# Kernel optimization log

Measured on AMD Instinct MI355X. Metric: run time of the kernel, lower is better.

## Reference

```python
import jax, jax.numpy as jnp
import numpy as np

B, N, IN, E, OUT = 4, 128, 256, 128, 128
EPS = 1e-5
NEG = -1.0e9


def _ln(x, s, o):
    m = x.mean(-1, keepdims=True)
    v = ((x - m) ** 2).mean(-1, keepdims=True)
    return s * jax.lax.rsqrt(v + EPS) * (x - m) + o


def setup_inputs() -> dict:
    key = jax.random.key(0)
    ks = jax.random.split(key, 30)

    def w(k, i, o):
        return (jax.random.normal(k, (i, o), jnp.float32) / np.sqrt(i)).astype(jnp.float32)

    z_dense = jax.random.normal(ks[0], (B, N, IN), jnp.float32)
    e_dense = jax.random.normal(ks[1], (B, N, N, E), jnp.float32)
    graph_fts = jax.random.normal(ks[2], (B, IN // 2), jnp.float32)
    lengths = jax.random.randint(ks[3], (B,), N // 2, N + 1)
    mask = jnp.arange(N)[None, :] < lengths[:, None]  # (B,N) bool
    adj = jax.random.uniform(ks[4], (B, N, N)) < 0.3
    adj = (adj | jnp.eye(N, dtype=bool)[None]) & mask[:, :, None] & mask[:, None, :]
    return dict(
        z_dense=z_dense, e_dense=e_dense, graph_fts=graph_fts, mask=mask, adj_mat=adj,
        Wt1=w(ks[5], IN, 8), Wt2=w(ks[6], IN, 8), Wt3=w(ks[7], IN, 8),
        We1=w(ks[8], E, 8), We2=w(ks[9], E, 8), We3=w(ks[10], E, 8),
        Wg=w(ks[11], IN // 2, 8),
        Wm1=w(ks[12], IN, OUT), Wm2=w(ks[13], IN, OUT), Wme=w(ks[14], E, OUT), Wmg=w(ks[15], E, OUT),
        ln1_s=jnp.ones((OUT,), jnp.float32), ln1_o=jnp.zeros((OUT,), jnp.float32),
        Wmlp1=w(ks[16], OUT, OUT),
        ln2_s=jnp.ones((OUT,), jnp.float32), ln2_o=jnp.zeros((OUT,), jnp.float32),
        Wmlp2=w(ks[17], OUT, OUT),
        WU1=w(ks[18], IN, OUT), WU2=w(ks[19], OUT, OUT), WU3=w(ks[20], 8, OUT),
        lnf_s=jnp.ones((OUT,), jnp.float32), lnf_o=jnp.zeros((OUT,), jnp.float32),
    )


def reference(z_dense, e_dense, graph_fts, mask, adj_mat,
              Wt1, Wt2, Wt3, We1, We2, We3, Wg,
              Wm1, Wm2, Wme, Wmg,
              ln1_s, ln1_o, Wmlp1, ln2_s, ln2_o, Wmlp2,
              WU1, WU2, WU3, lnf_s, lnf_o):
    mN = mask[..., None]  # (B,N,1)
    # --- triplet messages ---
    tri_1 = jnp.where(mN, z_dense @ Wt1, 0.0)  # (B,N,8)
    tri_2 = jnp.where(mN, z_dense @ Wt2, 0.0)
    tri_3 = jnp.where(mN, z_dense @ Wt3, 0.0)
    tri_e1 = e_dense @ We1  # (B,N,N,8)
    tri_e2 = e_dense @ We2
    tri_e3 = e_dense @ We3
    tri_g = graph_fts @ Wg  # (B,8)
    # (B,N,N,N,8) 7-way broadcast sum (axes: b, i, j, k)
    tri = (tri_1[:, :, None, None, :] + tri_2[:, None, :, None, :] + tri_3[:, None, None, :, :]
           + tri_e1[:, :, :, None, :] + tri_e2[:, :, None, :, :] + tri_e3[:, None, :, :, :]
           + tri_g[:, None, None, None, :])
    msk_tri = mask[:, None, None, :] | mask[:, None, :, None] | mask[:, :, None, None]
    tri = jnp.where(msk_tri[..., None], tri, NEG)
    tri_pooled = tri.max(axis=1)  # (B,N,N,8) -- max over first node axis
    tri_msgs = jax.nn.relu(tri_pooled @ WU3)  # (B,N,N,OUT)

    # --- pairwise messages ---
    msg_1 = jnp.where(mN, z_dense @ Wm1, 0.0)  # (B,N,OUT)
    msg_2 = jnp.where(mN, z_dense @ Wm2, 0.0)
    msg_e = jnp.where(adj_mat[..., None], e_dense @ Wme, 0.0)  # (B,N,N,OUT)
    msg_g = graph_fts @ Wmg  # (B,OUT)
    msgs = msg_1[:, None, :, :] + msg_2[:, :, None, :] + msg_e + msg_g[:, None, None, :]
    # M[-1]: [LN, ReLU, Linear] x2
    x = jax.nn.relu(_ln(msgs, ln1_s, ln1_o)) @ Wmlp1
    x = jax.nn.relu(_ln(x, ln2_s, ln2_o)) @ Wmlp2
    msgs = jnp.where(adj_mat[..., None], x, NEG).max(axis=1)  # (B,N,OUT)

    ret = _ln(z_dense @ WU1 + msgs @ WU2, lnf_s, lnf_o)  # (B,N,OUT)
    return ret, msgs, tri_msgs
```

## Files before the change

### kernel.cpp

```cpp
#include <hip/hip_runtime.h>

#define BN   4
#define NN   128
#define INF  256
#define EF   128
#define OUTF 128
#define EPSF 1e-5f
#define NEGF -998244352.0f

typedef __attribute__((ext_vector_type(8))) short short8;
typedef __attribute__((ext_vector_type(4))) float f32x4;

#define MFMA16(a, b, c) __builtin_amdgcn_mfma_f32_16x16x32_bf16(a, b, c, 0, 0, 0)

__device__ __forceinline__ unsigned short f2bf(float f) {
    unsigned u = __float_as_uint(f);
    u += 0x7fffu + ((u >> 16) & 1u);
    return (unsigned short)(u >> 16);
}
__device__ __forceinline__ unsigned pack2(float a, float b) {
    return (unsigned)f2bf(a) | ((unsigned)f2bf(b) << 16);
}

constexpr size_t TRI1 = 0;
constexpr size_t TRI2 = 4096;
constexpr size_t TRI3 = 8192;
constexpr size_t MSG1 = 12288;
constexpr size_t MSG2 = 77824;
constexpr size_t ZWU1 = 143360;
constexpr size_t TRIG = 208896;
constexpr size_t MSGG = 209920;
constexpr size_t E1T  = 210944;
constexpr size_t E2T  = 735232;
constexpr size_t E3N  = 1259520;
constexpr size_t PREPF = 1914880;

constexpr int W1T_OFF  = 0;
constexpr int W2T_OFF  = 16384;
constexpr int WMET_OFF = 32768;

constexpr size_t O_RET = 0;
constexpr size_t O_MSG = 65536;
constexpr size_t O_TRI = 131072;

__device__ __forceinline__ int detect_int(const void* mask) {
    const unsigned char* m = (const unsigned char*)mask;
    return (m[1] | m[2] | m[3]) == 0 ? 1 : 0;
}
__device__ __forceinline__ bool rdbool(const void* p, size_t idx, int isInt) {
    if (isInt) return ((const int*)p)[idx] != 0;
    return ((const unsigned char*)p)[idx] != 0;
}

__global__ __launch_bounds__(256, 4) void k_pre(
    const float* __restrict__ z, const float* __restrict__ e, const void* __restrict__ mask,
    const float* __restrict__ Wt1, const float* __restrict__ Wt2, const float* __restrict__ Wt3,
    const float* __restrict__ Wm1, const float* __restrict__ Wm2, const float* __restrict__ WU1,
    const float* __restrict__ g, const float* __restrict__ Wg, const float* __restrict__ Wmg,
    const float* __restrict__ W1, const float* __restrict__ W2, const float* __restrict__ Wme,
    const float* __restrict__ We1, const float* __restrict__ We2, const float* __restrict__ We3,
    float* __restrict__ ws, unsigned short* __restrict__ prep)
{
    int bx = blockIdx.x, tid = threadIdx.x;
    __shared__ __align__(16) unsigned char smem[128 * 136 * 2];

    if (bx < 512) {
        unsigned short* Ab = (unsigned short*)smem;
        int bi = bx;
        int b = bi >> 7, i = bi & 127;
        int lane = tid & 63, w = tid >> 6, q = lane >> 4, n = lane & 15;
        {
            int half = lane >> 5, c4 = (lane & 31) * 4;
            #pragma unroll
            for (int it = 0; it < 16; it++) {
                int row = 32 * w + 2 * it + half;
                float4 v = *(const float4*)(e + (size_t)bi * 16384 + (size_t)row * 128 + c4);
                unsigned* dst = (unsigned*)&Ab[row * 136 + c4];
                dst[0] = pack2(v.x, v.y);
                dst[1] = pack2(v.z, v.w);
            }
        }
        float t1v;
        {
            int c = lane & 7, kk = lane >> 3;
            const float* zr = z + (size_t)bi * INF;
            float s = 0.f;
            #pragma unroll
            for (int m = 0; m < 32; m++) s = fmaf(zr[kk * 32 + m], Wt1[(kk * 32 + m) * 8 + c], s);
            s += __shfl_xor(s, 8, 64);
            s += __shfl_xor(s, 16, 64);
            s += __shfl_xor(s, 32, 64);
            int isInt = detect_int(mask);
            t1v = rdbool(mask, bi, isInt) ? s : 0.f;
        }
        short8 bfrag[4][2];
        {
            #pragma unroll
            for (int t = 0; t < 2; t++) {
                int col = 16 * t + n;
                const float* Wsel = (col < 8) ? We1 : (col < 16 ? We2 : We3);
                int csel = col & 7;
                float mval = (col < 24) ? 1.f : 0.f;
                #pragma unroll
                for (int ks = 0; ks < 4; ks++) {
                    union { short8 s; unsigned short u[8]; } tmp;
                    #pragma unroll
                    for (int jj = 0; jj < 8; jj++) {
                        int k = ks * 32 + q * 8 + jj;
                        tmp.u[jj] = f2bf(Wsel[k * 8 + csel] * mval);
                    }
                    bfrag[ks][t] = tmp.s;
                }
            }
        }
        __builtin_amdgcn_wave_barrier();

        f32x4 ac2[2][2];
        #pragma unroll
        for (int rt = 0; rt < 2; rt++)
            #pragma unroll
            for (int t = 0; t < 2; t++) ac2[rt][t] = 0.f;
        #pragma unroll
        for (int ks = 0; ks < 4; ks++) {
            int k0 = ks * 32 + q * 8;
            short8 a0 = *(const short8*)&Ab[(32 * w + n) * 136 + k0];
            short8 a1 = *(const short8*)&Ab[(32 * w + 16 + n) * 136 + k0];
            #pragma unroll
            for (int t = 0; t < 2; t++) {
                ac2[0][t] = MFMA16(a0, bfrag[ks][t], ac2[0][t]);
                ac2[1][t] = MFMA16(a1, bfrag[ks][t], ac2[1][t]);
            }
        }
        #pragma unroll
        for (int rt = 0; rt < 2; rt++)
            #pragma unroll
            for (int reg = 0; reg < 4; reg++) {
                int row = 32 * w + 16 * rt + 4 * q + reg;
                float v0 = ac2[rt][0][reg];
                if (n < 8) ws[E1T + ((size_t)(b * 128 + row) * 128 + i) * 8 + n] = v0 + t1v;
                else       ws[E2T + ((size_t)(b * 128 + row) * 128 + i) * 8 + (n - 8)] = v0;
                if (n < 8) ws[E3N + ((size_t)bi * 128 + row) * 8 + n] = ac2[rt][1][reg];
            }
        return;
    }
    if (bx < 1024) {
        int bn = bx - 512;
        int isInt = detect_int(mask);
        float* zr = (float*)smem;
        zr[tid] = z[(size_t)bn * INF + tid];
        __syncthreads();
        float mk = rdbool(mask, bn, isInt) ? 1.f : 0.f;
        for (int idx = tid; idx < 408; idx += 256) {
            const float* W; int c; size_t dst; int width; bool msk;
            if (idx < 8)        { W = Wt1; c = idx;       dst = TRI1 + (size_t)bn * 8;   width = 8;   msk = true;  }
            else if (idx < 16)  { W = Wt2; c = idx - 8;   dst = TRI2 + (size_t)bn * 8;   width = 8;   msk = true;  }
            else if (idx < 24)  { W = Wt3; c = idx - 16;  dst = TRI3 + (size_t)bn * 8;   width = 8;   msk = true;  }
            else if (idx < 152) { W = Wm1; c = idx - 24;  dst = MSG1 + (size_t)bn * 128; width = 128; msk = true;  }
            else if (idx < 280) { W = Wm2; c = idx - 152; dst = MSG2 + (size_t)bn * 128; width = 128; msk = true;  }
            else                { W = WU1; c = idx - 280; dst = ZWU1 + (size_t)bn * 128; width = 128; msk = false; }
            float a0 = 0.f, a1 = 0.f;
            #pragma unroll 8
            for (int k = 0; k < INF; k += 2) {
                a0 += zr[k] * W[k * width + c];
                a1 += zr[k + 1] * W[(k + 1) * width + c];
            }
            float acc = a0 + a1;
            ws[dst + c] = msk ? acc * mk : acc;
        }
        return;
    }
    if (bx < 1028) {
        int b = bx - 1024;
        float* gr = (float*)smem;
        if (tid < 128) gr[tid] = g[b * 128 + tid];
        __syncthreads();
        if (tid < 8) {
            float a = 0.f;
            for (int k = 0; k < 128; k++) a += gr[k] * Wg[k * 8 + tid];
            ws[TRIG + b * 8 + tid] = a;
        } else if (tid >= 128) {
            int c = tid - 128;
            float a = 0.f;
            for (int k = 0; k < 128; k++) a += gr[k] * Wmg[k * 128 + c];
            ws[MSGG + b * 128 + c] = a;
        }
        return;
    }
    {
        int idx = (bx - 1028) * 256 + tid;
        const float* W = (idx < 16384) ? W1 : (idx < 32768 ? W2 : Wme);
        int local = idx & 16383;
        int f = local >> 3, jj = local & 7;
        int lane = f & 63, fg = f >> 6;
        int t = fg & 7, ks = fg >> 3;
        int n = lane & 15, q = lane >> 4;
        int row = 16 * t + n;
        int k = ks * 32 + q * 8 + jj;
        prep[idx] = f2bf(W[k * 128 + row]);
    }
}

#define PAIR_GEMM(OFF) do {                                                            \
    short8 btc[8], btn[8];                                                             \
    _Pragma("unroll")                                                                  \
    for (int t = 0; t < 8; t++)                                                        \
        btc[t] = *(const short8*)&prep[(OFF) + ((0 * 8 + t) * 64 + lane) * 8];         \
    _Pragma("unroll")                                                                  \
    for (int ks = 0; ks < 4; ks++) {                                                   \
        int kf = ks * 32 + q * 8;                                                      \
        short8 a0 = *(const short8*)&Ab[(32 * w + n) * 136 + kf];                      \
        short8 a1 = *(const short8*)&Ab[(32 * w + 16 + n) * 136 + kf];                 \
        if (ks < 3) {                                                                  \
            _Pragma("unroll")                                                          \
            for (int t = 0; t < 8; t++)                                                \
                btn[t] = *(const short8*)&prep[(OFF) + (((ks + 1) * 8 + t) * 64 + lane) * 8]; \
        }                                                                              \
        _Pragma("unroll")                                                              \
        for (int t = 0; t < 8; t++) {                                                  \
            acc[0][t] = MFMA16(a0, btc[t], acc[0][t]);                                 \
            acc[1][t] = MFMA16(a1, btc[t], acc[1][t]);                                 \
        }                                                                              \
        if (ks < 3) {                                                                  \
            _Pragma("unroll")                                                          \
            for (int t = 0; t < 8; t++) btc[t] = btn[t];                               \
        }                                                                              \
    }                                                                                  \
} while (0)

__global__ __launch_bounds__(256, 3) void k_main(
    const float* __restrict__ e, const void* __restrict__ mask, const void* __restrict__ adj,
    const float* __restrict__ ln1s, const float* __restrict__ ln1o,
    const float* __restrict__ ln2s, const float* __restrict__ ln2o,
    const unsigned short* __restrict__ prep, const float* __restrict__ WU3,
    float* __restrict__ ws, float* __restrict__ out)
{
    int bx = blockIdx.x, tid = threadIdx.x;
    __shared__ __align__(16) unsigned char smem[128 * 136 * 2 + 2048];
    int lane = tid & 63, w = tid >> 6, q = lane >> 4, n = lane & 15;
    int isInt = detect_int(mask);

    if (bx < 256) {
        int g = bx;
        int j0 = ((g >> 3) & 7) * 16, k0 = (g & 7) * 16, b = g >> 6;
        int wi = w >> 1, wc = w & 1;
        int tj = lane >> 3, tk = lane & 7;
        int col4 = (tid & 31) * 4, rowgrp = tid >> 5;

        int lenb;
        {
            unsigned long long m0 = __ballot(rdbool(mask, (size_t)b * 128 + lane, isInt));
            unsigned long long m1 = __ballot(rdbool(mask, (size_t)b * 128 + 64 + lane, isInt));
            lenb = __popcll(m0) + __popcll(m1);
        }
        bool needU = (j0 + 15 >= lenb) && (k0 + 15 >= lenb);

        float* Pb = (float*)smem + w * 1152;
        float* Qb = Pb + 576;

        f32x4 aM[2][2];
        #pragma unroll
        for (int jj = 0; jj < 2; jj++)
            #pragma unroll
            for (int kk = 0; kk < 2; kk++) aM[jj][kk] = NEGF;

        if (!needU) {
            for (int ch = 0; ch < 8; ch++) {
                int ibase = wi * 64 + ch * 8;
                #pragma unroll
                for (int r = 0; r < 2; r++) {
                    int f = r * 64 + lane;
                    int jr = f >> 3, ii = f & 7;
                    f32x4 pv = *(const f32x4*)(ws + E1T + (size_t)(b * 128 + j0 + jr) * 1024 + (ibase + ii) * 8 + wc * 4);
                    f32x4 qv = *(const f32x4*)(ws + E2T + (size_t)(b * 128 + k0 + jr) * 1024 + (ibase + ii) * 8 + wc * 4);
                    *(f32x4*)(Pb + jr * 36 + ii * 4) = pv;
                    *(f32x4*)(Qb + jr * 36 + ii * 4) = qv;
                }
                __builtin_amdgcn_wave_barrier();
                #pragma unroll
                for (int ii = 0; ii < 8; ii++) {
                    f32x4 p0 = *(const f32x4*)(Pb + tj * 36 + ii * 4);
                    f32x4 p1 = *(const f32x4*)(Pb + (tj + 8) * 36 + ii * 4);
                    f32x4 q0 = *(const f32x4*)(Qb + tk * 36 + ii * 4);
                    f32x4 q1 = *(const f32x4*)(Qb + (tk + 8) * 36 + ii * 4);
                    aM[0][0] = __builtin_elementwise_max(aM[0][0], p0 + q0);
                    aM[0][1] = __builtin_elementwise_max(aM[0][1], p0 + q1);
                    aM[1][0] = __builtin_elementwise_max(aM[1][0], p1 + q0);
                    aM[1][1] = __builtin_elementwise_max(aM[1][1], p1 + q1);
                }
            }
        } else {
            f32x4 aU[2][2];
// ... 51 lines not shown
        float4 wvr[8];
        #pragma unroll
        for (int c = 0; c < 8; c++) wvr[c] = *(const float4*)(WU3 + c * 128 + col4);

        if (wi == 0) {
            #pragma unroll
            for (int jj = 0; jj < 2; jj++)
                #pragma unroll
                for (int kk = 0; kk < 2; kk++) {
                    int p = (tj + 8 * jj) * 16 + (tk + 8 * kk);
                    #pragma unroll
                    for (int cc = 0; cc < 4; cc++)
                        pooled[(wc * 4 + cc) * 260 + p] = aM[jj][kk][cc];
                }
        }
        __syncthreads();
        if (wi == 1) {
            const float* tg = ws + TRIG + (size_t)b * 8 + wc * 4;
            #pragma unroll
            for (int jj = 0; jj < 2; jj++)
                #pragma unroll
                for (int kk = 0; kk < 2; kk++) {
                    int jv = j0 + tj + 8 * jj, kv = k0 + tk + 8 * kk;
                    const float* t2 = ws + TRI2 + (size_t)(b * 128 + jv) * 8 + wc * 4;
                    const float* t3 = ws + TRI3 + (size_t)(b * 128 + kv) * 8 + wc * 4;
                    const float* e3 = ws + E3N + ((size_t)(b * 128 + jv) * 128 + kv) * 8 + wc * 4;
                    int p = (tj + 8 * jj) * 16 + (tk + 8 * kk);
                    #pragma unroll
                    for (int cc = 0; cc < 4; cc++) {
                        int idx = (wc * 4 + cc) * 260 + p;
                        pooled[idx] = fmaxf(pooled[idx], aM[jj][kk][cc]) + t2[cc] + t3[cc] + e3[cc] + tg[cc];
                    }
                }
        }
        __syncthreads();
        #pragma unroll
        for (int pass = 0; pass < 32; pass++) {
            int p = pass * 8 + rowgrp;
            float4 s = { 0.f, 0.f, 0.f, 0.f };
            #pragma unroll
            for (int c = 0; c < 8; c++) {
                float pv = pooled[c * 260 + p];
                s.x += pv * wvr[c].x; s.y += pv * wvr[c].y;
                s.z += pv * wvr[c].z; s.w += pv * wvr[c].w;
            }
            s.x = fmaxf(s.x, 0.f); s.y = fmaxf(s.y, 0.f);
            s.z = fmaxf(s.z, 0.f); s.w = fmaxf(s.w, 0.f);
            int pj = p >> 4, pk = p & 15;
            *(float4*)(out + O_TRI + ((size_t)(b * 128 + j0 + pj) * 128 + (k0 + pk)) * 128 + col4) = s;
        }
        return;
    }

    unsigned short* Ab = (unsigned short*)smem;
    float* pw = (float*)(smem + 128 * 136 * 2);
    int bj = bx - 256;
    int b = bj >> 7, j = bj & 127;

    int lenb;
    {
        unsigned long long m0 = __ballot(rdbool(mask, (size_t)b * 128 + lane, isInt));
        unsigned long long m1 = __ballot(rdbool(mask, (size_t)b * 128 + 64 + lane, isInt));
        lenb = __popcll(m0) + __popcll(m1);
    }
    if (j >= lenb) {
        if (tid < 128) out[O_MSG + (size_t)bj * 128 + tid] = NEGF;
        return;
    }

    float colmax[8];
    #pragma unroll
    for (int t = 0; t < 8; t++) colmax[t] = NEGF;

    bool waveActive = (32 * w) < lenb;
    if (waveActive) {
        {
            int half = lane >> 5, c4 = (lane & 31) * 4;
            #pragma unroll
            for (int it = 0; it < 16; it++) {
                int row = 32 * w + 2 * it + half;
                float4 v = *(const float4*)(e + (((size_t)b * 128 + row) * 128 + j) * 128 + c4);
                unsigned* dst = (unsigned*)&Ab[row * 136 + c4];
                dst[0] = pack2(v.x, v.y);
                dst[1] = pack2(v.z, v.w);
            }
        }
        __builtin_amdgcn_wave_barrier();

        f32x4 acc[2][8];
        #pragma unroll
        for (int rt = 0; rt < 2; rt++)
            #pragma unroll
            for (int t = 0; t < 8; t++) acc[rt][t] = 0.f;

        PAIR_GEMM(WMET_OFF);

        float msum[8];
        #pragma unroll
        for (int t = 0; t < 8; t++)
            msum[t] = ws[MSG1 + (size_t)bj * 128 + 16 * t + n] + ws[MSGG + (size_t)b * 128 + 16 * t + n];
        float adjm[2][4];
        float rs[2][4], rss[2][4];
        #pragma unroll
        for (int rt = 0; rt < 2; rt++)
            #pragma unroll
            for (int reg = 0; reg < 4; reg++) {
                int row = 32 * w + 16 * rt + 4 * q + reg;
                bool av = rdbool(adj, ((size_t)b * 128 + row) * 128 + j, isInt);
                adjm[rt][reg] = av ? 1.f : 0.f;
                float s = 0.f, ssq = 0.f;
                #pragma unroll
                for (int t = 0; t < 8; t++) {
                    float v = acc[rt][t][reg] * adjm[rt][reg]
                            + ws[MSG2 + ((size_t)b * 128 + row) * 128 + 16 * t + n] + msum[t];
                    acc[rt][t][reg] = v;
                    s += v; ssq += v * v;
                }
                rs[rt][reg] = s; rss[rt][reg] = ssq;
            }
        #pragma unroll
        for (int d = 1; d < 16; d <<= 1) {
            #pragma unroll
            for (int rt = 0; rt < 2; rt++)
                #pragma unroll
                for (int reg = 0; reg < 4; reg++) {
                    rs[rt][reg]  += __shfl_xor(rs[rt][reg], d, 64);
                    rss[rt][reg] += __shfl_xor(rss[rt][reg], d, 64);
                }
        }
        {
            float s1v[8], o1v[8];
            #pragma unroll
            for (int t = 0; t < 8; t++) { s1v[t] = ln1s[16 * t + n]; o1v[t] = ln1o[16 * t + n]; }
            #pragma unroll
            for (int rt = 0; rt < 2; rt++)
                #pragma unroll
                for (int reg = 0; reg < 4; reg++) {
                    float mu = rs[rt][reg] * (1.f / 128);
                    float inv = rsqrtf(rss[rt][reg] * (1.f / 128) - mu * mu + EPSF);
                    int row = 32 * w + 16 * rt + 4 * q + reg;
                    #pragma unroll
                    for (int t = 0; t < 8; t++) {
                        float v = fmaxf(s1v[t] * inv * (acc[rt][t][reg] - mu) + o1v[t], 0.f);
                        Ab[row * 136 + 16 * t + n] = f2bf(v);
                    }
                }
        }
        __builtin_amdgcn_wave_barrier();

        #pragma unroll
        for (int rt = 0; rt < 2; rt++)
            #pragma unroll
            for (int t = 0; t < 8; t++) acc[rt][t] = 0.f;
        PAIR_GEMM(W1T_OFF);
        #pragma unroll
        for (int rt = 0; rt < 2; rt++)
            #pragma unroll
            for (int reg = 0; reg < 4; reg++) {
                float s = 0.f, ssq = 0.f;
                #pragma unroll
                for (int t = 0; t < 8; t++) { float v = acc[rt][t][reg]; s += v; ssq += v * v; }
                rs[rt][reg] = s; rss[rt][reg] = ssq;
            }
        #pragma unroll
        for (int d = 1; d < 16; d <<= 1) {
            #pragma unroll
            for (int rt = 0; rt < 2; rt++)
                #pragma unroll
                for (int reg = 0; reg < 4; reg++) {
                    rs[rt][reg]  += __shfl_xor(rs[rt][reg], d, 64);
                    rss[rt][reg] += __shfl_xor(rss[rt][reg], d, 64);
                }
        }
        {
            float s2v[8], o2v[8];
            #pragma unroll
            for (int t = 0; t < 8; t++) { s2v[t] = ln2s[16 * t + n]; o2v[t] = ln2o[16 * t + n]; }
            #pragma unroll
            for (int rt = 0; rt < 2; rt++)
                #pragma unroll
                for (int reg = 0; reg < 4; reg++) {
                    float mu = rs[rt][reg] * (1.f / 128);
                    float inv = rsqrtf(rss[rt][reg] * (1.f / 128) - mu * mu + EPSF);
                    int row = 32 * w + 16 * rt + 4 * q + reg;
                    #pragma unroll
                    for (int t = 0; t < 8; t++) {
                        float v = fmaxf(s2v[t] * inv * (acc[rt][t][reg] - mu) + o2v[t], 0.f);
                        Ab[row * 136 + 16 * t + n] = f2bf(v);
                    }
                }
        }
        __builtin_amdgcn_wave_barrier();

        #pragma unroll
        for (int rt = 0; rt < 2; rt++)
            #pragma unroll
            for (int t = 0; t < 8; t++) acc[rt][t] = 0.f;
        PAIR_GEMM(W2T_OFF);

        #pragma unroll
        for (int rt = 0; rt < 2; rt++)
            #pragma unroll
            for (int reg = 0; reg < 4; reg++) {
                if (adjm[rt][reg] > 0.f) {
                    #pragma unroll
                    for (int t = 0; t < 8; t++) colmax[t] = fmaxf(colmax[t], acc[rt][t][reg]);
                }
            }
    }
    #pragma unroll
    for (int t = 0; t < 8; t++) {
        colmax[t] = fmaxf(colmax[t], __shfl_xor(colmax[t], 16, 64));
        colmax[t] = fmaxf(colmax[t], __shfl_xor(colmax[t], 32, 64));
    }
    if (lane < 16) {
        #pragma unroll
        for (int t = 0; t < 8; t++) pw[w * 128 + 16 * t + lane] = colmax[t];
    }
    __syncthreads();
    if (tid < 128) {
        float mx = fmaxf(fmaxf(pw[tid], pw[128 + tid]), fmaxf(pw[256 + tid], pw[384 + tid]));
        out[O_MSG + (size_t)bj * 128 + tid] = mx;
    }
}

__global__ __launch_bounds__(128) void k_final(
    const float* __restrict__ ws, const float* __restrict__ WU2,
    const float* __restrict__ lnfs, const float* __restrict__ lnfo,
    float* __restrict__ out)
{
    int bn = blockIdx.x, tid = threadIdx.x;
    __shared__ float mrow[128];
    __shared__ float red[4];
    mrow[tid] = out[O_MSG + (size_t)bn * 128 + tid];
    __syncthreads();
    float y = ws[ZWU1 + (size_t)bn * 128 + tid];
    float a0 = 0.f, a1 = 0.f;
    #pragma unroll 8
    for (int k = 0; k < 128; k += 2) {
        a0 = fmaf(mrow[k], WU2[k * 128 + tid], a0);
        a1 = fmaf(mrow[k + 1], WU2[(k + 1) * 128 + tid], a1);
    }
    y += a0 + a1;
    float s = y, ss = y * y;
    for (int d = 1; d < 64; d <<= 1) { s += __shfl_xor(s, d, 64); ss += __shfl_xor(ss, d, 64); }
    if ((tid & 63) == 0) { red[(tid >> 6) * 2] = s; red[(tid >> 6) * 2 + 1] = ss; }
    __syncthreads();
    float S = red[0] + red[2], SS = red[1] + red[3];
    float m_ = S * (1.f / 128), v_ = SS * (1.f / 128) - m_ * m_;
    float r = rsqrtf(v_ + EPSF);
    out[O_RET + (size_t)bn * 128 + tid] = lnfs[tid] * r * (y - m_) + lnfo[tid];
}

extern "C" void kernel_launch(void* const* d_in, const int* in_sizes, int n_in,
                              void* d_out, int out_size, void* d_ws, size_t ws_size,
                              hipStream_t stream)
{
    const float* z    = (const float*)d_in[0];
    const float* e    = (const float*)d_in[1];
    const float* gf   = (const float*)d_in[2];
    const void*  mask = d_in[3];
    const void*  adj  = d_in[4];
    const float* Wt1 = (const float*)d_in[5];
    const float* Wt2 = (const float*)d_in[6];
    const float* Wt3 = (const float*)d_in[7];
    const float* We1 = (const float*)d_in[8];
    const float* We2 = (const float*)d_in[9];
    const float* We3 = (const float*)d_in[10];
    const float* Wg  = (const float*)d_in[11];
    const float* Wm1 = (const float*)d_in[12];
    const float* Wm2 = (const float*)d_in[13];
    const float* Wme = (const float*)d_in[14];
    const float* Wmg = (const float*)d_in[15];
    const float* ln1s = (const float*)d_in[16];
    const float* ln1o = (const float*)d_in[17];
    const float* W1   = (const float*)d_in[18];
    const float* ln2s = (const float*)d_in[19];
    const float* ln2o = (const float*)d_in[20];
    const float* W2   = (const float*)d_in[21];
    const float* WU1  = (const float*)d_in[22];
    const float* WU2  = (const float*)d_in[23];
    const float* WU3  = (const float*)d_in[24];
    const float* lnfs = (const float*)d_in[25];
    const float* lnfo = (const float*)d_in[26];
    float* out = (float*)d_out;
    float* ws  = (float*)d_ws;
    unsigned short* prep = (unsigned short*)(ws + PREPF);

    hipLaunchKernelGGL(k_pre, dim3(1220), dim3(256), 0, stream,
                       z, e, mask, Wt1, Wt2, Wt3, Wm1, Wm2, WU1, gf, Wg, Wmg,
                       W1, W2, Wme, We1, We2, We3, ws, prep);
    hipLaunchKernelGGL(k_main, dim3(768), dim3(256), 0, stream,
                       e, mask, adj, ln1s, ln1o, ln2s, ln2o, prep, WU3, ws, out);
    hipLaunchKernelGGL(k_final, dim3(512), dim3(128), 0, stream,
                       ws, WU2, lnfs, lnfo, out);
}
```

Measured before the change: 180.7 us.

## Rebalance stages: move edge triplet GEMM into main kernel, merge tri and final

The edge-projection (tri_e1/e2/e3) MFMA work moves out of the pre kernel into the main pairwise kernel, with even blocks doing it and odd blocks doing the message MLP. This lets both streams of e_dense reads run in one launch. The triplet pooling and final LayerNorm stage are merged into a new post kernel that processes two rows per 256-thread block. The aim is to shorten the serial pre stage and improve load balance across stages, at the cost of a more heterogeneous main kernel whose block types differ in register and LDS needs.

Result: slower. 205.0 us (+13.4%).

```diff
diff --git a/kernel.cpp b/kernel.cpp
--- a/kernel.cpp
+++ b/kernel.cpp
@@ -53,100 +53,19 @@
 }
 
 __global__ __launch_bounds__(256, 4) void k_pre(
-    const float* __restrict__ z, const float* __restrict__ e, const void* __restrict__ mask,
+    const float* __restrict__ z, const void* __restrict__ mask,
     const float* __restrict__ Wt1, const float* __restrict__ Wt2, const float* __restrict__ Wt3,
     const float* __restrict__ Wm1, const float* __restrict__ Wm2, const float* __restrict__ WU1,
     const float* __restrict__ g, const float* __restrict__ Wg, const float* __restrict__ Wmg,
     const float* __restrict__ W1, const float* __restrict__ W2, const float* __restrict__ Wme,
-    const float* __restrict__ We1, const float* __restrict__ We2, const float* __restrict__ We3,
     float* __restrict__ ws, unsigned short* __restrict__ prep)
 {
     int bx = blockIdx.x, tid = threadIdx.x;
-    __shared__ __align__(16) unsigned char smem[128 * 136 * 2];
+    __shared__ float zr[256];
 
     if (bx < 512) {
-        unsigned short* Ab = (unsigned short*)smem;
-        int bi = bx;
-        int b = bi >> 7, i = bi & 127;
-        int lane = tid & 63, w = tid >> 6, q = lane >> 4, n = lane & 15;
-        {
-            int half = lane >> 5, c4 = (lane & 31) * 4;
-            #pragma unroll
-            for (int it = 0; it < 16; it++) {
-                int row = 32 * w + 2 * it + half;
-                float4 v = *(const float4*)(e + (size_t)bi * 16384 + (size_t)row * 128 + c4);
-                unsigned* dst = (unsigned*)&Ab[row * 136 + c4];
-                dst[0] = pack2(v.x, v.y);
-                dst[1] = pack2(v.z, v.w);
-            }
-        }
-        float t1v;
-        {
-            int c = lane & 7, kk = lane >> 3;
-            const float* zr = z + (size_t)bi * INF;
-            float s = 0.f;
-            #pragma unroll
-            for (int m = 0; m < 32; m++) s = fmaf(zr[kk * 32 + m], Wt1[(kk * 32 + m) * 8 + c], s);
-            s += __shfl_xor(s, 8, 64);
-            s += __shfl_xor(s, 16, 64);
-            s += __shfl_xor(s, 32, 64);
-            int isInt = detect_int(mask);
-            t1v = rdbool(mask, bi, isInt) ? s : 0.f;
-        }
-        short8 bfrag[4][2];
-        {
-            #pragma unroll
-            for (int t = 0; t < 2; t++) {
-                int col = 16 * t + n;
-                const float* Wsel = (col < 8) ? We1 : (col < 16 ? We2 : We3);
-                int csel = col & 7;
-                float mval = (col < 24) ? 1.f : 0.f;
-                #pragma unroll
-                for (int ks = 0; ks < 4; ks++) {
-                    union { short8 s; unsigned short u[8]; } tmp;
-                    #pragma unroll
-                    for (int jj = 0; jj < 8; jj++) {
-                        int k = ks * 32 + q * 8 + jj;
-                        tmp.u[jj] = f2bf(Wsel[k * 8 + csel] * mval);
-                    }
-                    bfrag[ks][t] = tmp.s;
-                }
-            }
-        }
-        __builtin_amdgcn_wave_barrier();
-
-        f32x4 ac2[2][2];
-        #pragma unroll
-        for (int rt = 0; rt < 2; rt++)
-            #pragma unroll
-            for (int t = 0; t < 2; t++) ac2[rt][t] = 0.f;
-        #pragma unroll
-        for (int ks = 0; ks < 4; ks++) {
-            int k0 = ks * 32 + q * 8;
-            short8 a0 = *(const short8*)&Ab[(32 * w + n) * 136 + k0];
-            short8 a1 = *(const short8*)&Ab[(32 * w + 16 + n) * 136 + k0];
-            #pragma unroll
-            for (int t = 0; t < 2; t++) {
-                ac2[0][t] = MFMA16(a0, bfrag[ks][t], ac2[0][t]);
-                ac2[1][t] = MFMA16(a1, bfrag[ks][t], ac2[1][t]);
-            }
-        }
-        #pragma unroll
-        for (int rt = 0; rt < 2; rt++)
-            #pragma unroll
-            for (int reg = 0; reg < 4; reg++) {
-                int row = 32 * w + 16 * rt + 4 * q + reg;
-                float v0 = ac2[rt][0][reg];
-                if (n < 8) ws[E1T + ((size_t)(b * 128 + row) * 128 + i) * 8 + n] = v0 + t1v;
-                else       ws[E2T + ((size_t)(b * 128 + row) * 128 + i) * 8 + (n - 8)] = v0;
-                if (n < 8) ws[E3N + ((size_t)bi * 128 + row) * 8 + n] = ac2[rt][1][reg];
-            }
-        return;
-    }
-    if (bx < 1024) {
-        int bn = bx - 512;
+        int bn = bx;
         int isInt = detect_int(mask);
-        float* zr = (float*)smem;
         zr[tid] = z[(size_t)bn * INF + tid];
         __syncthreads();
         float mk = rdbool(mask, bn, isInt) ? 1.f : 0.f;
@@ -169,25 +88,24 @@
         }
         return;
     }
-    if (bx < 1028) {
-        int b = bx - 1024;
-        float* gr = (float*)smem;
-        if (tid < 128) gr[tid] = g[b * 128 + tid];
+    if (bx < 516) {
+        int b = bx - 512;
+        if (tid < 128) zr[tid] = g[b * 128 + tid];
         __syncthreads();
         if (tid < 8) {
             float a = 0.f;
-            for (int k = 0; k < 128; k++) a += gr[k] * Wg[k * 8 + tid];
+            for (int k = 0; k < 128; k++) a += zr[k] * Wg[k * 8 + tid];
             ws[TRIG + b * 8 + tid] = a;
         } else if (tid >= 128) {
             int c = tid - 128;
             float a = 0.f;
-            for (int k = 0; k < 128; k++) a += gr[k] * Wmg[k * 128 + c];
+            for (int k = 0; k < 128; k++) a += zr[k] * Wmg[k * 128 + c];
             ws[MSGG + b * 128 + c] = a;
         }
         return;
     }
     {
-        int idx = (bx - 1028) * 256 + tid;
+        int idx = (bx - 516) * 256 + tid;
         const float* W = (idx < 16384) ? W1 : (idx < 32768 ? W2 : Wme);
         int local = idx & 16383;
         int f = local >> 3, jj = local & 7;
@@ -227,16 +145,306 @@
     }                                                                                  \
 } while (0)
 
-__global__ __launch_bounds__(256, 3) void k_main(
-    const float* __restrict__ e, const void* __restrict__ mask, const void* __restrict__ adj,
+__global__ __launch_bounds__(256, 3) void k_mid(
+    const float* __restrict__ z, const float* __restrict__ e,
+    const void* __restrict__ mask, const void* __restrict__ adj,
+    const float* __restrict__ Wt1,
+    const float* __restrict__ We1, const float* __restrict__ We2, const float* __restrict__ We3,
     const float* __restrict__ ln1s, const float* __restrict__ ln1o,
     const float* __restrict__ ln2s, const float* __restrict__ ln2o,
-    const unsigned short* __restrict__ prep, const float* __restrict__ WU3,
+    const unsigned short* __restrict__ prep,
     float* __restrict__ ws, float* __restrict__ out)
 {
     int bx = blockIdx.x, tid = threadIdx.x;
     __shared__ __align__(16) unsigned char smem[128 * 136 * 2 + 2048];
     int lane = tid & 63, w = tid >> 6, q = lane >> 4, n = lane & 15;
+    int isInt = detect_int(mask);
+
+    if ((bx & 1) == 0) {
+        unsigned short* Ab = (unsigned short*)smem;
+        int bi = bx >> 1;
+        int b = bi >> 7, i = bi & 127;
+        {
+            int half = lane >> 5, c4 = (lane & 31) * 4;
+            #pragma unroll
+            for (int it = 0; it < 16; it++) {
+                int row = 32 * w + 2 * it + half;
+                float4 v = *(const float4*)(e + (size_t)bi * 16384 + (size_t)row * 128 + c4);
+                unsigned* dst = (unsigned*)&Ab[row * 136 + c4];
+                dst[0] = pack2(v.x, v.y);
+                dst[1] = pack2(v.z, v.w);
+            }
+        }
+        float t1v;
+        {
+            int c = lane & 7, kk = lane >> 3;
+            const float* zr = z + (size_t)bi * INF;
+            float s = 0.f;
+            #pragma unroll
+            for (int m = 0; m < 32; m++) s = fmaf(zr[kk * 32 + m], Wt1[(kk * 32 + m) * 8 + c], s);
+            s += __shfl_xor(s, 8, 64);
+            s += __shfl_xor(s, 16, 64);
+            s += __shfl_xor(s, 32, 64);
+            t1v = rdbool(mask, bi, isInt) ? s : 0.f;
+        }
+        short8 bfrag[4][2];
+        {
+            #pragma unroll
+            for (int t = 0; t < 2; t++) {
+                int col = 16 * t + n;
+                const float* Wsel = (col < 8) ? We1 : (col < 16 ? We2 : We3);
+                int csel = col & 7;
+                float mval = (col < 24) ? 1.f : 0.f;
+                #pragma unroll
+                for (int ks = 0; ks < 4; ks++) {
+                    union { short8 s; unsigned short u[8]; } tmp;
+                    #pragma unroll
+                    for (int jj = 0; jj < 8; jj++) {
+                        int k = ks * 32 + q * 8 + jj;
+                        tmp.u[jj] = f2bf(Wsel[k * 8 + csel] * mval);
+                    }
+                    bfrag[ks][t] = tmp.s;
+                }
+            }
+        }
+        __builtin_amdgcn_wave_barrier();
+
+        f32x4 ac2[2][2];
+        #pragma unroll
+        for (int rt = 0; rt < 2; rt++)
+            #pragma unroll
+            for (int t = 0; t < 2; t++) ac2[rt][t] = 0.f;
+        #pragma unroll
+        for (int ks = 0; ks < 4; ks++) {
+            int k0 = ks * 32 + q * 8;
+            short8 a0 = *(const short8*)&Ab[(32 * w + n) * 136 + k0];
+            short8 a1 = *(const short8*)&Ab[(32 * w + 16 + n) * 136 + k0];
+            #pragma unroll
+            for (int t = 0; t < 2; t++) {
+                ac2[0][t] = MFMA16(a0, bfrag[ks][t], ac2[0][t]);
+                ac2[1][t] = MFMA16(a1, bfrag[ks][t], ac2[1][t]);
+            }
+        }
+        #pragma unroll
+        for (int rt = 0; rt < 2; rt++)
+            #pragma unroll
+            for (int reg = 0; reg < 4; reg++) {
+                int row = 32 * w + 16 * rt + 4 * q + reg;
+                float v0 = ac2[rt][0][reg];
+                if (n < 8) ws[E1T + ((size_t)(b * 128 + row) * 128 + i) * 8 + n] = v0 + t1v;
+                else       ws[E2T + ((size_t)(b * 128 + row) * 128 + i) * 8 + (n - 8)] = v0;
+                if (n < 8) ws[E3N + ((size_t)bi * 128 + row) * 8 + n] = ac2[rt][1][reg];
+            }
+        return;
+    }
+
+    unsigned short* Ab = (unsigned short*)smem;
+    float* pw = (float*)(smem + 128 * 136 * 2);
+    int bj = bx >> 1;
+    int b = bj >> 7, j = bj & 127;
+
+    int lenb;
+    {
+        unsigned long long m0 = __ballot(rdbool(mask, (size_t)b * 128 + lane, isInt));
+        unsigned long long m1 = __ballot(rdbool(mask, (size_t)b * 128 + 64 + lane, isInt));
+        lenb = __popcll(m0) + __popcll(m1);
+    }
+    if (j >= lenb) {
+        if (tid < 128) out[O_MSG + (size_t)bj * 128 + tid] = NEGF;
+        return;
+    }
+
+    float colmax[8];
+    #pragma unroll
+    for (int t = 0; t < 8; t++) colmax[t] = NEGF;
+
+    bool waveActive = (32 * w) < lenb;
+    if (waveActive) {
+        short8 btc[8];
+        #pragma unroll
+        for (int t = 0; t < 8; t++)
+            btc[t] = *(const short8*)&prep[WMET_OFF + ((0 * 8 + t) * 64 + lane) * 8];
+        {
+            int half = lane >> 5, c4 = (lane & 31) * 4;
+            #pragma unroll
+            for (int it = 0; it < 16; it++) {
+                int row = 32 * w + 2 * it + half;
+                float4 v = *(const float4*)(e + (((size_t)b * 128 + row) * 128 + j) * 128 + c4);
+                unsigned* dst = (unsigned*)&Ab[row * 136 + c4];
+                dst[0] = pack2(v.x, v.y);
+                dst[1] = pack2(v.z, v.w);
+            }
+        }
+        __builtin_amdgcn_wave_barrier();
+
+        f32x4 acc[2][8];
+        #pragma unroll
+        for (int rt = 0; rt < 2; rt++)
+            #pragma unroll
+            for (int t = 0; t < 8; t++) acc[rt][t] = 0.f;
+
+        {
+            short8 btn[8];
+            #pragma unroll
+            for (int ks = 0; ks < 4; ks++) {
+                int kf = ks * 32 + q * 8;
+                short8 a0 = *(const short8*)&Ab[(32 * w + n) * 136 + kf];
+                short8 a1 = *(const short8*)&Ab[(32 * w + 16 + n) * 136 + kf];
+                if (ks < 3) {
+                    #pragma unroll
+                    for (int t = 0; t < 8; t++)
+                        btn[t] = *(const short8*)&prep[WMET_OFF + (((ks + 1) * 8 + t) * 64 + lane) * 8];
+                }
+                #pragma unroll
+                for (int t = 0; t < 8; t++) {
+                    acc[0][t] = MFMA16(a0, btc[t], acc[0][t]);
+                    acc[1][t] = MFMA16(a1, btc[t], acc[1][t]);
+                }
+                if (ks < 3) {
+                    #pragma unroll
+                    for (int t = 0; t < 8; t++) btc[t] = btn[t];
+                }
+            }
+        }
+
+        float msum[8];
+        #pragma unroll
+        for (int t = 0; t < 8; t++)
+            msum[t] = ws[MSG1 + (size_t)bj * 128 + 16 * t + n] + ws[MSGG + (size_t)b * 128 + 16 * t + n];
+        float adjm[2][4];
+        float rs[2][4], rss[2][4];
+        #pragma unroll
+        for (int rt = 0; rt < 2; rt++)
+            #pragma unroll
+            for (int reg = 0; reg < 4; reg++) {
+                int row = 32 * w + 16 * rt + 4 * q + reg;
+                bool av = rdbool(adj, ((size_t)b * 128 + row) * 128 + j, isInt);
+                adjm[rt][reg] = av ? 1.f : 0.f;
+                float s = 0.f, ssq = 0.f;
+                #pragma unroll
+                for (int t = 0; t < 8; t++) {
+                    float v = acc[rt][t][reg] * adjm[rt][reg]
+                            + ws[MSG2 + ((size_t)b * 128 + row) * 128 + 16 * t + n] + msum[t];
+                    acc[rt][t][reg] = v;
+                    s += v; ssq += v * v;
+                }
+                rs[rt][reg] = s; rss[rt][reg] = ssq;
+            }
+        #pragma unroll
+        for (int d = 1; d < 16; d <<= 1) {
+            #pragma unroll
+            for (int rt = 0; rt < 2; rt++)
+                #pragma unroll
+                for (int reg = 0; reg < 4; reg++) {
+                    rs[rt][reg]  += __shfl_xor(rs[rt][reg], d, 64);
+                    rss[rt][reg] += __shfl_xor(rss[rt][reg], d, 64);
+                }
+        }
+        {
+            float s1v[8], o1v[8];
+            #pragma unroll
+            for (int t = 0; t < 8; t++) { s1v[t] = ln1s[16 * t + n]; o1v[t] = ln1o[16 * t + n]; }
+            #pragma unroll
+            for (int rt = 0; rt < 2; rt++)
+                #pragma unroll
+                for (int reg = 0; reg < 4; reg++) {
+                    float mu = rs[rt][reg] * (1.f / 128);
+                    float inv = rsqrtf(rss[rt][reg] * (1.f / 128) - mu * mu + EPSF);
+                    int row = 32 * w + 16 * rt + 4 * q + reg;
+                    #pragma unroll
+                    for (int t = 0; t < 8; t++) {
+                        float v = fmaxf(s1v[t] * inv * (acc[rt][t][reg] - mu) + o1v[t], 0.f);
+                        Ab[row * 136 + 16 * t + n] = f2bf(v);
+                    }
+                }
+        }
+        __builtin_amdgcn_wave_barrier();
+
+        #pragma unroll
+        for (int rt = 0; rt < 2; rt++)
+            #pragma unroll
+            for (int t = 0; t < 8; t++) acc[rt][t] = 0.f;
+        PAIR_GEMM(W1T_OFF);
+        #pragma unroll
+        for (int rt = 0; rt < 2; rt++)
+            #pragma unroll
+            for (int reg = 0; reg < 4; reg++) {
+                float s = 0.f, ssq = 0.f;
+                #pragma unroll
+                for (int t = 0; t < 8; t++) { float v = acc[rt][t][reg]; s += v; ssq += v * v; }
+                rs[rt][reg] = s; rss[rt][reg] = ssq;
+            }
+        #pragma unroll
+        for (int d = 1; d < 16; d <<= 1) {
+            #pragma unroll
+            for (int rt = 0; rt < 2; rt++)
+                #pragma unroll
+                for (int reg = 0; reg < 4; reg++) {
+                    rs[rt][reg]  += __shfl_xor(rs[rt][reg], d, 64);
+                    rss[rt][reg] += __shfl_xor(rss[rt][reg], d, 64);
+                }
+        }
+        {
+            float s2v[8], o2v[8];
+            #pragma unroll
+            for (int t = 0; t < 8; t++) { s2v[t] = ln2s[16 * t + n]; o2v[t] = ln2o[16 * t + n]; }
+            #pragma unroll
+            for (int rt = 0; rt < 2; rt++)
+                #pragma unroll
+                for (int reg = 0; reg < 4; reg++) {
+                    float mu = rs[rt][reg] * (1.f / 128);
+                    float inv = rsqrtf(rss[rt][reg] * (1.f / 128) - mu * mu + EPSF);
+                    int row = 32 * w + 16 * rt + 4 * q + reg;
+                    #pragma unroll
+                    for (int t = 0; t < 8; t++) {
+                        float v = fmaxf(s2v[t] * inv * (acc[rt][t][reg] - mu) + o2v[t], 0.f);
+                        Ab[row * 136 + 16 * t + n] = f2bf(v);
+                    }
+                }
+        }
+        __builtin_amdgcn_wave_barrier();
+
+        #pragma unroll
+        for (int rt = 0; rt < 2; rt++)
+            #pragma unroll
+            for (int t = 0; t < 8; t++) acc[rt][t] = 0.f;
+        PAIR_GEMM(W2T_OFF);
+
+        #pragma unroll
+        for (int rt = 0; rt < 2; rt++)
+            #pragma unroll
+            for (int reg = 0; reg < 4; reg++) {
+                if (adjm[rt][reg] > 0.f) {
+                    #pragma unroll
+                    for (int t = 0; t < 8; t++) colmax[t] = fmaxf(colmax[t], acc[rt][t][reg]);
+                }
+            }
+    }
+    #pragma unroll
+    for (int t = 0; t < 8; t++) {
+        colmax[t] = fmaxf(colmax[t], __shfl_xor(colmax[t], 16, 64));
+        colmax[t] = fmaxf(colmax[t], __shfl_xor(colmax[t], 32, 64));
+    }
+    if (lane < 16) {
+        #pragma unroll
+        for (int t = 0; t < 8; t++) pw[w * 128 + 16 * t + lane] = colmax[t];
+    }
+    __syncthreads();
+    if (tid < 128) {
+        float mx = fmaxf(fmaxf(pw[tid], pw[128 + tid]), fmaxf(pw[256 + tid], pw[384 + tid]));
+        out[O_MSG + (size_t)bj * 128 + tid] = mx;
+    }
+}
+
+__global__ __launch_bounds__(256, 4) void k_post(
+    const void* __restrict__ mask,
+    const float* __restrict__ WU3, const float* __restrict__ WU2,
+    const float* __restrict__ lnfs, const float* __restrict__ lnfo,
+    float* __restrict__ ws, float* __restrict__ out)
+{
+    int bx = blockIdx.x, tid = threadIdx.x;
+    __shared__ __align__(16) unsigned char smem[4 * 1152 * 4];
+    int lane = tid & 63, w = tid >> 6;
     int isInt = detect_int(mask);
 
     if (bx < 256) {
@@ -394,204 +602,31 @@
         return;
     }
 
-    unsigned short* Ab = (unsigned short*)smem;
-    float* pw = (float*)(smem + 128 * 136 * 2);
-    int bj = bx - 256;
-    int b = bj >> 7, j = bj & 127;
-
-    int lenb;
     {
-        unsigned long long m0 = __ballot(rdbool(mask, (size_t)b * 128 + lane, isInt));
-        unsigned long long m1 = __ballot(rdbool(mask, (size_t)b * 128 + 64 + lane, isInt));
-        lenb = __popcll(m0) + __popcll(m1);
-    }
-    if (j >= lenb) {
-        if (tid < 128) out[O_MSG + (size_t)bj * 128 + tid] = NEGF;
-        return;
-    }
-
-    float colmax[8];
-    #pragma unroll
-    for (int t = 0; t < 8; t++) colmax[t] = NEGF;
-
-    bool waveActive = (32 * w) < lenb;
-    if (waveActive) {
-        {
-            int half = lane >> 5, c4 = (lane & 31) * 4;
-            #pragma unroll
-            for (int it = 0; it < 16; it++) {
-                int row = 32 * w + 2 * it + half;
-                float4 v = *(const float4*)(e + (((size_t)b * 128 + row) * 128 + j) * 128 + c4);
-                unsigned* dst = (unsigned*)&Ab[row * 136 + c4];
-                dst[0] = pack2(v.x, v.y);
-                dst[1] = pack2(v.z, v.w);
-            }
-        }
-        __builtin_amdgcn_wave_barrier();
-
-        f32x4 acc[2][8];
-        #pragma unroll
-        for (int rt = 0; rt < 2; rt++)
-            #pragma unroll
-            for (int t = 0; t < 8; t++) acc[rt][t] = 0.f;
-
-        PAIR_GEMM(WMET_OFF);
-
-        float msum[8];
-        #pragma unroll
-        for (int t = 0; t < 8; t++)
-            msum[t] = ws[MSG1 + (size_t)bj * 128 + 16 * t + n] + ws[MSGG + (size_t)b * 128 + 16 * t + n];
-        float adjm[2][4];
-        float rs[2][4], rss[2][4];
-        #pragma unroll
-        for (int rt = 0; rt < 2; rt++)
-            #pragma unroll
-            for (int reg = 0; reg < 4; reg++) {
-                int row = 32 * w + 16 * rt + 4 * q + reg;
-                bool av = rdbool(adj, ((size_t)b * 128 + row) * 128 + j, isInt);
-                adjm[rt][reg] = av ? 1.f : 0.f;
-                float s = 0.f, ssq = 0.f;
-                #pragma unroll
-                for (int t = 0; t < 8; t++) {
-                    float v = acc[rt][t][reg] * adjm[rt][reg]
-                            + ws[MSG2 + ((size_t)b * 128 + row) * 128 + 16 * t + n] + msum[t];
-                    acc[rt][t][reg] = v;
-                    s += v; ssq += v * v;
-                }
-                rs[rt][reg] = s; rss[rt][reg] = ssq;
-            }
-        #pragma unroll
-        for (int d = 1; d < 16; d <<= 1) {
-            #pragma unroll
-            for (int rt = 0; rt < 2; rt++)
-                #pragma unroll
-                for (int reg = 0; reg < 4; reg++) {
-                    rs[rt][reg]  += __shfl_xor(rs[rt][reg], d, 64);
-                    rss[rt][reg] += __shfl_xor(rss[rt][reg], d, 64);
-                }
-        }
-        {
-            float s1v[8], o1v[8];
-            #pragma unroll
-            for (int t = 0; t < 8; t++) { s1v[t] = ln1s[16 * t + n]; o1v[t] = ln1o[16 * t + n]; }
-            #pragma unroll
-            for (int rt = 0; rt < 2; rt++)
-                #pragma unroll
-                for (int reg = 0; reg < 4; reg++) {
-                    float mu = rs[rt][reg] * (1.f / 128);
-                    float inv = rsqrtf(rss[rt][reg] * (1.f / 128) - mu * mu + EPSF);
-                    int row = 32 * w + 16 * rt + 4 * q + reg;
-                    #pragma unroll
-                    for (int t = 0; t < 8; t++) {
-                        float v = fmaxf(s1v[t] * inv * (acc[rt][t][reg] - mu) + o1v[t], 0.f);
-                        Ab[row * 136 + 16 * t + n] = f2bf(v);
-                    }
-                }
-        }
-        __builtin_amdgcn_wave_barrier();
-
-        #pragma unroll
-        for (int rt = 0; rt < 2; rt++)
-            #pragma unroll
-            for (int t = 0; t < 8; t++) acc[rt][t] = 0.f;
-        PAIR_GEMM(W1T_OFF);
-        #pragma unroll
-        for (int rt = 0; rt < 2; rt++)
-            #pragma unroll
-            for (int reg = 0; reg < 4; reg++) {
-                float s = 0.f, ssq = 0.f;
-                #pragma unroll
-                for (int t = 0; t < 8; t++) { float v = acc[rt][t][reg]; s += v; ssq += v * v; }
-                rs[rt][reg] = s; rss[rt][reg] = ssq;
-            }
-        #pragma unroll
-        for (int d = 1; d < 16; d <<= 1) {
-            #pragma unroll
-            for (int rt = 0; rt < 2; rt++)
-                #pragma unroll
-                for (int reg = 0; reg < 4; reg++) {
-                    rs[rt][reg]  += __shfl_xor(rs[rt][reg], d, 64);
-                    rss[rt][reg] += __shfl_xor(rss[rt][reg], d, 64);
-                }
-        }
-        {
-            float s2v[8], o2v[8];
-            #pragma unroll
-            for (int t = 0; t < 8; t++) { s2v[t] = ln2s[16 * t + n]; o2v[t] = ln2o[16 * t + n]; }
-            #pragma unroll
-            for (int rt = 0; rt < 2; rt++)
-                #pragma unroll
-                for (int reg = 0; reg < 4; reg++) {
-                    float mu = rs[rt][reg] * (1.f / 128);
-                    float inv = rsqrtf(rss[rt][reg] * (1.f / 128) - mu * mu + EPSF);
-                    int row = 32 * w + 16 * rt + 4 * q + reg;
-                    #pragma unroll
-                    for (int t = 0; t < 8; t++) {
-                        float v = fmaxf(s2v[t] * inv * (acc[rt][t][reg] - mu) + o2v[t], 0.f);
-                        Ab[row * 136 + 16 * t + n] = f2bf(v);
-                    }
-                }
-        }
-        __builtin_amdgcn_wave_barrier();
-
-        #pragma unroll
-        for (int rt = 0; rt < 2; rt++)
-            #pragma unroll
-            for (int t = 0; t < 8; t++) acc[rt][t] = 0.f;
-        PAIR_GEMM(W2T_OFF);
-
-        #pragma unroll
-        for (int rt = 0; rt < 2; rt++)
-            #pragma unroll
-            for (int reg = 0; reg < 4; reg++) {
-                if (adjm[rt][reg] > 0.f) {
-                    #pragma unroll
-                    for (int t = 0; t < 8; t++) colmax[t] = fmaxf(colmax[t], acc[rt][t][reg]);
-                }
-            }
-    }
-    #pragma unroll
-    for (int t = 0; t < 8; t++) {
-        colmax[t] = fmaxf(colmax[t], __shfl_xor(colmax[t], 16, 64));
-        colmax[t] = fmaxf(colmax[t], __shfl_xor(colmax[t], 32, 64));
-    }
-    if (lane < 16) {
-        #pragma unroll
-        for (int t = 0; t < 8; t++) pw[w * 128 + 16 * t + lane] = colmax[t];
-    }
-    __syncthreads();
-    if (tid < 128) {
-        float mx = fmaxf(fmaxf(pw[tid], pw[128 + tid]), fmaxf(pw[256 + tid], pw[384 + tid]));
-        out[O_MSG + (size_t)bj * 128 + tid] = mx;
-    }
-}
-
-__global__ __launch_bounds__(128) void k_final(
-    const float* __restrict__ ws, const float* __restrict__ WU2,
-    const float* __restrict__ lnfs, const float* __restrict__ lnfo,
-    float* __restrict__ out)
-{
-    int bn = blockIdx.x, tid = threadIdx.x;
-    __shared__ float mrow[128];
-    __shared__ float red[4];
-    mrow[tid] = out[O_MSG + (size_t)bn * 128 + tid];
-    __syncthreads();
-    float y = ws[ZWU1 + (size_t)bn * 128 + tid];
-    float a0 = 0.f, a1 = 0.f;
-    #pragma unroll 8
-    for (int k = 0; k < 128; k += 2) {
-        a0 = fmaf(mrow[k], WU2[k * 128 + tid], a0);
-        a1 = fmaf(mrow[k + 1], WU2[(k + 1) * 128 + tid], a1);
-    }
-    y += a0 + a1;
-    float s = y, ss = y * y;
-    for (int d = 1; d < 64; d <<= 1) { s += __shfl_xor(s, d, 64); ss += __shfl_xor(ss, d, 64); }
-    if ((tid & 63) == 0) { red[(tid >> 6) * 2] = s; red[(tid >> 6) * 2 + 1] = ss; }
-    __syncthreads();
-    float S = red[0] + red[2], SS = red[1] + red[3];
-    float m_ = S * (1.f / 128), v_ = SS * (1.f / 128) - m_ * m_;
-    float r = rsqrtf(v_ + EPSF);
-    out[O_RET + (size_t)bn * 128 + tid] = lnfs[tid] * r * (y - m_) + lnfo[tid];
+        float* mrow = (float*)smem;
+        float* red  = (float*)(smem + 1024);
+        int grp = tid >> 7, t7 = tid & 127;
+        int bn = (bx - 256) * 2 + grp;
+        mrow[grp * 128 + t7] = out[O_MSG + (size_t)bn * 128 + t7];
+        __syncthreads();
+        float y = ws[ZWU1 + (size_t)bn * 128 + t7];
+        float a0 = 0.f, a1 = 0.f;
+        const float* mr = mrow + grp * 128;
+        #pragma unroll 8
+        for (int k = 0; k < 128; k += 2) {
+            a0 = fmaf(mr[k], WU2[k * 128 + t7], a0);
+            a1 = fmaf(mr[k + 1], WU2[(k + 1) * 128 + t7], a1);
+        }
+        y += a0 + a1;
+        float s = y, ss = y * y;
+        for (int d = 1; d < 64; d <<= 1) { s += __shfl_xor(s, d, 64); ss += __shfl_xor(ss, d, 64); }
+        if ((tid & 63) == 0) { red[grp * 4 + (t7 >> 6) * 2] = s; red[grp * 4 + (t7 >> 6) * 2 + 1] = ss; }
+        __syncthreads();
+        float S = red[grp * 4 + 0] + red[grp * 4 + 2], SS = red[grp * 4 + 1] + red[grp * 4 + 3];
+        float m_ = S * (1.f / 128), v_ = SS * (1.f / 128) - m_ * m_;
+        float r = rsqrtf(v_ + EPSF);
+        out[O_RET + (size_t)bn * 128 + t7] = lnfs[t7] * r * (y - m_) + lnfo[t7];
+    }
 }
 
 extern "C" void kernel_launch(void* const* d_in, const int* in_sizes, int n_in,
@@ -629,11 +664,12 @@
     float* ws  = (float*)d_ws;
     unsigned short* prep = (unsigned short*)(ws + PREPF);
 
-    hipLaunchKernelGGL(k_pre, dim3(1220), dim3(256), 0, stream,
-                       z, e, mask, Wt1, Wt2, Wt3, Wm1, Wm2, WU1, gf, Wg, Wmg,
-                       W1, W2, Wme, We1, We2, We3, ws, prep);
-    hipLaunchKernelGGL(k_main, dim3(768), dim3(256), 0, stream,
-                       e, mask, adj, ln1s, ln1o, ln2s, ln2o, prep, WU3, ws, out);
-    hipLaunchKernelGGL(k_final, dim3(512), dim3(128), 0, stream,
-                       ws, WU2, lnfs, lnfo, out);
-}
+    hipLaunchKernelGGL(k_pre, dim3(708), dim3(256), 0, stream,
+                       z, mask, Wt1, Wt2, Wt3, Wm1, Wm2, WU1, gf, Wg, Wmg,
+                       W1, W2, Wme, ws, prep);
+    hipLaunchKernelGGL(k_mid, dim3(1024), dim3(256), 0, stream,
+                       z, e, mask, adj, Wt1, We1, We2, We3,
+                       ln1s, ln1o, ln2s, ln2o, prep, ws, out);
+    hipLaunchKernelGGL(k_post, dim3(512), dim3(256), 0, stream,
+                       mask, WU3, WU2, lnfs, lnfo, ws, out);
+}
```

## Stage pairwise-MLP weights in LDS with register prefetch of the next matrix

Applied to the files above, without the earlier changes.

Each pairwise GEMM previously streamed its bf16 weight fragments from global memory per wave, so all four waves re-read the same 32KB matrix. The weights are now copied cooperatively into a 32KB LDS buffer, and the next matrix is prefetched into registers while the current GEMM runs. Waves then read B fragments from LDS. This adds block-wide barriers, 8 uint4 prefetch registers per thread and more shared memory, and lowers launch bounds from 3 to 2 blocks per CU, which can reduce occupancy.

Measured after the change: 196.4 us. 1.09x slower.

```diff
diff --git a/kernel.cpp b/kernel.cpp
--- a/kernel.cpp
+++ b/kernel.cpp
@@ -200,34 +200,34 @@
     }
 }
 
-#define PAIR_GEMM(OFF) do {                                                            \
-    short8 btc[8], btn[8];                                                             \
-    _Pragma("unroll")                                                                  \
-    for (int t = 0; t < 8; t++)                                                        \
-        btc[t] = *(const short8*)&prep[(OFF) + ((0 * 8 + t) * 64 + lane) * 8];         \
-    _Pragma("unroll")                                                                  \
-    for (int ks = 0; ks < 4; ks++) {                                                   \
-        int kf = ks * 32 + q * 8;                                                      \
-        short8 a0 = *(const short8*)&Ab[(32 * w + n) * 136 + kf];                      \
-        short8 a1 = *(const short8*)&Ab[(32 * w + 16 + n) * 136 + kf];                 \
-        if (ks < 3) {                                                                  \
-            _Pragma("unroll")                                                          \
-            for (int t = 0; t < 8; t++)                                                \
-                btn[t] = *(const short8*)&prep[(OFF) + (((ks + 1) * 8 + t) * 64 + lane) * 8]; \
-        }                                                                              \
-        _Pragma("unroll")                                                              \
-        for (int t = 0; t < 8; t++) {                                                  \
-            acc[0][t] = MFMA16(a0, btc[t], acc[0][t]);                                 \
-            acc[1][t] = MFMA16(a1, btc[t], acc[1][t]);                                 \
-        }                                                                              \
-        if (ks < 3) {                                                                  \
-            _Pragma("unroll")                                                          \
-            for (int t = 0; t < 8; t++) btc[t] = btn[t];                               \
-        }                                                                              \
-    }                                                                                  \
+#define PAIR_GEMM_L do {                                                       \
+    _Pragma("unroll")                                                          \
+    for (int ks = 0; ks < 4; ks++) {                                           \
+        int kf = ks * 32 + q * 8;                                              \
+        short8 a0 = *(const short8*)&Ab[(32 * w + n) * 136 + kf];              \
+        short8 a1 = *(const short8*)&Ab[(32 * w + 16 + n) * 136 + kf];         \
+        _Pragma("unroll")                                                      \
+        for (int t = 0; t < 8; t++) {                                          \
+            short8 bt = *(const short8*)&Wl[((ks * 8 + t) * 64 + lane) * 8];   \
+            acc[0][t] = MFMA16(a0, bt, acc[0][t]);                             \
+            acc[1][t] = MFMA16(a1, bt, acc[1][t]);                             \
+        }                                                                      \
+    }                                                                          \
 } while (0)
 
-__global__ __launch_bounds__(256, 3) void k_main(
+#define W_ISSUE(OFF) do {                                                      \
+    const uint4* s_ = (const uint4*)(prep + (OFF));                            \
+    _Pragma("unroll")                                                          \
+    for (int r = 0; r < 8; r++) wpref[r] = s_[r * 256 + tid];                  \
+} while (0)
+
+#define W_WRITE() do {                                                         \
+    uint4* d_ = (uint4*)Wl;                                                    \
+    _Pragma("unroll")                                                          \
+    for (int r = 0; r < 8; r++) d_[r * 256 + tid] = wpref[r];                  \
+} while (0)
+
+__global__ __launch_bounds__(256, 2) void k_main(
     const float* __restrict__ e, const void* __restrict__ mask, const void* __restrict__ adj,
     const float* __restrict__ ln1s, const float* __restrict__ ln1o,
     const float* __restrict__ ln2s, const float* __restrict__ ln2o,
@@ -235,7 +235,7 @@
     float* __restrict__ ws, float* __restrict__ out)
 {
     int bx = blockIdx.x, tid = threadIdx.x;
-    __shared__ __align__(16) unsigned char smem[128 * 136 * 2 + 2048];
+    __shared__ __align__(16) unsigned char smem[128 * 136 * 2 + 2048 + 32768];
     int lane = tid & 63, w = tid >> 6, q = lane >> 4, n = lane & 15;
     int isInt = detect_int(mask);
 
@@ -396,6 +396,7 @@
 
     unsigned short* Ab = (unsigned short*)smem;
     float* pw = (float*)(smem + 128 * 136 * 2);
+    unsigned short* Wl = (unsigned short*)(smem + 128 * 136 * 2 + 2048);
     int bj = bx - 256;
     int b = bj >> 7, j = bj & 127;
 
@@ -410,38 +411,41 @@
         return;
     }
 
+    bool waveActive = (32 * w) < lenb;
+    uint4 wpref[8];
+    W_ISSUE(WMET_OFF);
+    if (waveActive) {
+        int half = lane >> 5, c4 = (lane & 31) * 4;
+        #pragma unroll
+        for (int it = 0; it < 16; it++) {
+            int row = 32 * w + 2 * it + half;
+            float4 v = *(const float4*)(e + (((size_t)b * 128 + row) * 128 + j) * 128 + c4);
+            unsigned* dst = (unsigned*)&Ab[row * 136 + c4];
+            dst[0] = pack2(v.x, v.y);
+            dst[1] = pack2(v.z, v.w);
+        }
+    }
+    W_WRITE();
+    __syncthreads();
+
     float colmax[8];
     #pragma unroll
     for (int t = 0; t < 8; t++) colmax[t] = NEGF;
-
-    bool waveActive = (32 * w) < lenb;
+    float adjm[2][4];
+    f32x4 acc[2][8];
+
+    W_ISSUE(W1T_OFF);
     if (waveActive) {
-        {
-            int half = lane >> 5, c4 = (lane & 31) * 4;
-            #pragma unroll
-            for (int it = 0; it < 16; it++) {
-                int row = 32 * w + 2 * it + half;
-                float4 v = *(const float4*)(e + (((size_t)b * 128 + row) * 128 + j) * 128 + c4);
-                unsigned* dst = (unsigned*)&Ab[row * 136 + c4];
-                dst[0] = pack2(v.x, v.y);
-                dst[1] = pack2(v.z, v.w);
-            }
-        }
-        __builtin_amdgcn_wave_barrier();
-
-        f32x4 acc[2][8];
         #pragma unroll
         for (int rt = 0; rt < 2; rt++)
             #pragma unroll
             for (int t = 0; t < 8; t++) acc[rt][t] = 0.f;
-
-        PAIR_GEMM(WMET_OFF);
+        PAIR_GEMM_L;
 
         float msum[8];
         #pragma unroll
         for (int t = 0; t < 8; t++)
             msum[t] = ws[MSG1 + (size_t)bj * 128 + 16 * t + n] + ws[MSGG + (size_t)b * 128 + 16 * t + n];
-        float adjm[2][4];
         float rs[2][4], rss[2][4];
         #pragma unroll
         for (int rt = 0; rt < 2; rt++)
@@ -488,13 +492,20 @@
                     }
                 }
         }
-        __builtin_amdgcn_wave_barrier();
-
+    }
+    __syncthreads();
+    W_WRITE();
+    __syncthreads();
+
+    W_ISSUE(W2T_OFF);
+    if (waveActive) {
         #pragma unroll
         for (int rt = 0; rt < 2; rt++)
             #pragma unroll
             for (int t = 0; t < 8; t++) acc[rt][t] = 0.f;
-        PAIR_GEMM(W1T_OFF);
+        PAIR_GEMM_L;
+
+        float rs[2][4], rss[2][4];
         #pragma unroll
         for (int rt = 0; rt < 2; rt++)
             #pragma unroll
@@ -532,13 +543,17 @@
                     }
                 }
         }
-        __builtin_amdgcn_wave_barrier();
-
+    }
+    __syncthreads();
+    W_WRITE();
+    __syncthreads();
+
+    if (waveActive) {
         #pragma unroll
         for (int rt = 0; rt < 2; rt++)
             #pragma unroll
             for (int t = 0; t < 8; t++) acc[rt][t] = 0.f;
-        PAIR_GEMM(W2T_OFF);
+        PAIR_GEMM_L;
 
         #pragma unroll
         for (int rt = 0; rt < 2; rt++)
```
